# Performance work log

Measured on AMD Instinct MI355X. Metric: run time of the kernel, lower is better.

The kernel has to match this reference:

```python
import jax, jax.numpy as jnp
import numpy as np

DIM = 2048
NC = 12  # n_components (hard-coded in module)
EPS = 1e-5


def setup_inputs() -> dict:
    key = jax.random.key(0)
    ks = jax.random.split(key, 8)
    s = lambda fan_in: 1.0 / np.sqrt(fan_in)
    return {
        "x": jax.random.normal(ks[0], (8, 4096, DIM), dtype=jnp.float32),
        "Wp": jax.random.uniform(ks[1], (DIM, NC), jnp.float32, -s(DIM), s(DIM)),
        "bp": jax.random.uniform(ks[2], (NC,), jnp.float32, -s(DIM), s(DIM)),
        "Wv": jax.random.uniform(ks[3], (DIM, NC), jnp.float32, -s(DIM), s(DIM)),
        "bv": jax.random.uniform(ks[4], (NC,), jnp.float32, -s(DIM), s(DIM)),
        "Wi": jax.random.uniform(ks[5], (NC * NC, DIM), jnp.float32, -s(NC * NC), s(NC * NC)),
        "bi": jax.random.uniform(ks[6], (DIM,), jnp.float32, -s(NC * NC), s(NC * NC)),
        "gamma": jnp.ones((DIM,), jnp.float32),
        "beta": jnp.zeros((DIM,), jnp.float32),
    }


def reference(x, Wp, bp, Wv, bv, Wi, bi, gamma, beta):
    B, N, D = x.shape
    pos = x @ Wp + bp                      # [B,N,12]
    vel = x @ Wv + bv                      # [B,N,12]
    inter = jnp.einsum('bni,bnj->bnij', pos, vel).reshape(B, N, NC * NC)
    inter = inter @ Wi + bi                # [B,N,D]
    y = x + inter
    mu = jnp.mean(y, axis=-1, keepdims=True)
    var = jnp.mean(jnp.square(y - mu), axis=-1, keepdims=True)
    return (y - mu) * jax.lax.rsqrt(var + EPS) * gamma + beta
```

## Files before the change

### kernel.cpp

```cpp
#include <hip/hip_runtime.h>

#define D 2048
#define KPAD 160
#define PSTR 168
#define MTILE 16
#define THREADS 512

typedef __attribute__((ext_vector_type(8))) short bf16x8;
typedef __attribute__((ext_vector_type(4))) float f32x4;

__device__ inline unsigned short f2bf(float f) {
  unsigned int u = __float_as_uint(f);
  u += 0x7fffu + ((u >> 16) & 1u);
  return (unsigned short)(u >> 16);
}

__global__ __launch_bounds__(256) void prep_wpv(const float* __restrict__ Wp,
                                                const float* __restrict__ Wv,
                                                unsigned short* __restrict__ Wpvt) {
  int idx = blockIdx.x * 256 + threadIdx.x;
  int n = idx >> 11, k = idx & 2047;
  float v = 0.f;
  if (n < 12) v = Wp[k * 12 + n];
  else if (n < 24) v = Wv[k * 12 + (n - 12)];
  Wpvt[idx] = f2bf(v);
}

__global__ __launch_bounds__(256) void prep_wi(const float* __restrict__ Wi,
                                               unsigned short* __restrict__ Wit) {
  int idx = blockIdx.x * 256 + threadIdx.x;
  int n = idx / KPAD, k = idx - n * KPAD;
  float v = (k < 144) ? Wi[k * 2048 + n] : 0.f;
  Wit[idx] = f2bf(v);
}

__global__ __launch_bounds__(THREADS, 4) void gil_fused(
    const float* __restrict__ x, const float* __restrict__ bp,
    const float* __restrict__ bv, const float* __restrict__ bi,
    const float* __restrict__ gamma, const float* __restrict__ beta,
    const unsigned short* __restrict__ Wpvt, const unsigned short* __restrict__ Wit,
    float* __restrict__ out) {
  __shared__ float sred[8][MTILE][36];
  __shared__ __align__(16) unsigned short sP[MTILE][PSTR];
  __shared__ float spart[8][MTILE][2];
  __shared__ float sstat[MTILE][2];

  const int t = threadIdx.x;
  const int rowbase = blockIdx.x * MTILE;
  const int wave = t >> 6, lane = t & 63;
  const int lm = lane & 15, quad = lane >> 4;

  {
    const float* xr = x + (size_t)(rowbase + lm) * D + wave * 256;
    const unsigned short* b0 = Wpvt + (size_t)lm * D + wave * 256;
    const unsigned short* b1 = Wpvt + (size_t)(16 + lm) * D + wave * 256;
    f32x4 acc0 = {0.f, 0.f, 0.f, 0.f}, acc1 = {0.f, 0.f, 0.f, 0.f};
#pragma unroll
    for (int kk = 0; kk < 8; ++kk) {
      int k0 = kk * 32 + quad * 8;
      f32x4 v0 = *(const f32x4*)(xr + k0);
      f32x4 v1 = *(const f32x4*)(xr + k0 + 4);
      bf16x8 a;
#pragma unroll
      for (int e = 0; e < 4; ++e) {
        a[e]     = (short)f2bf(v0[e]);
        a[4 + e] = (short)f2bf(v1[e]);
      }
      bf16x8 w0 = *(const bf16x8*)(b0 + k0);
      bf16x8 w1 = *(const bf16x8*)(b1 + k0);
      acc0 = __builtin_amdgcn_mfma_f32_16x16x32_bf16(a, w0, acc0, 0, 0, 0);
      acc1 = __builtin_amdgcn_mfma_f32_16x16x32_bf16(a, w1, acc1, 0, 0, 0);
    }
#pragma unroll
    for (int rg = 0; rg < 4; ++rg) {
      sred[wave][quad * 4 + rg][lm]      = acc0[rg];
      sred[wave][quad * 4 + rg][16 + lm] = acc1[rg];
    }
  }
  __syncthreads();

  {
    int m = t >> 5, n = t & 31;
    float pv = 0.f;
#pragma unroll
    for (int w = 0; w < 8; ++w) pv += sred[w][m][n];
    if (n < 12) pv += bp[n];
    else if (n < 24) pv += bv[n - 12];
#pragma unroll
    for (int kk = 0; kk < 5; ++kk) {
      int k = n + 32 * kk;
      int i = k / 12, j = k - i * 12;
      float a = __shfl(pv, i, 32);
      float b = __shfl(pv, 12 + j, 32);
      sP[m][k] = f2bf((k < 144) ? a * b : 0.f);
    }
  }
  __syncthreads();

  f32x4 accv[16];
  {
    bf16x8 bf[5];
#pragma unroll
    for (int kc = 0; kc < 5; ++kc)
      bf[kc] = *(const bf16x8*)&sP[lm][kc * 32 + quad * 8];
#pragma unroll
    for (int nt = 0; nt < 16; ++nt) {
      const unsigned short* wb = Wit + (size_t)(wave * 256 + nt * 16 + lm) * KPAD;
      f32x4 acc = {0.f, 0.f, 0.f, 0.f};
#pragma unroll
      for (int kc = 0; kc < 5; ++kc) {
        bf16x8 wv = *(const bf16x8*)(wb + kc * 32 + quad * 8);
        acc = __builtin_amdgcn_mfma_f32_16x16x32_bf16(wv, bf[kc], acc, 0, 0, 0);
      }
      accv[nt] = acc;
    }
  }

  float s = 0.f, ss = 0.f;
  {
    const float* xrow = x + (size_t)(rowbase + lm) * D;
#pragma unroll
    for (int nt = 0; nt < 16; ++nt) {
      int d0 = wave * 256 + nt * 16 + quad * 4;
      f32x4 bi4 = *(const f32x4*)(bi + d0);
      f32x4 x4  = *(const f32x4*)(xrow + d0);
#pragma unroll
      for (int rg = 0; rg < 4; ++rg) {
        float y = accv[nt][rg] + bi4[rg] + x4[rg];
        accv[nt][rg] = y;
        s += y;
        ss += y * y;
      }
    }
    s += __shfl_xor(s, 16); ss += __shfl_xor(ss, 16);
    s += __shfl_xor(s, 32); ss += __shfl_xor(ss, 32);
    if (lane < 16) { spart[wave][lm][0] = s; spart[wave][lm][1] = ss; }
  }
  __syncthreads();
  if (t < MTILE) {
    float su = 0.f, sq = 0.f;
#pragma unroll
    for (int w = 0; w < 8; ++w) { su += spart[w][t][0]; sq += spart[w][t][1]; }
    float mu = su * (1.f / D);
    float var = sq * (1.f / D) - mu * mu;
    sstat[t][0] = mu;
    sstat[t][1] = rsqrtf(var + 1e-5f);
  }
  __syncthreads();

  {
    float mu = sstat[lm][0], rs = sstat[lm][1];
    float* orow = out + (size_t)(rowbase + lm) * D;
#pragma unroll
    for (int nt = 0; nt < 16; ++nt) {
      int d0 = wave * 256 + nt * 16 + quad * 4;
      f32x4 g4  = *(const f32x4*)(gamma + d0);
      f32x4 be4 = *(const f32x4*)(beta + d0);
      f32x4 o;
#pragma unroll
      for (int rg = 0; rg < 4; ++rg)
        o[rg] = (accv[nt][rg] - mu) * rs * g4[rg] + be4[rg];
      *(f32x4*)(orow + d0) = o;
    }
  }
}

extern "C" void kernel_launch(void* const* d_in, const int* in_sizes, int n_in,
                              void* d_out, int out_size, void* d_ws, size_t ws_size,
                              hipStream_t stream) {
  const float* x     = (const float*)d_in[0];
  const float* Wp    = (const float*)d_in[1];
  const float* bp    = (const float*)d_in[2];
  const float* Wv    = (const float*)d_in[3];
  const float* bv    = (const float*)d_in[4];
  const float* Wi    = (const float*)d_in[5];
  const float* bi    = (const float*)d_in[6];
  const float* gamma = (const float*)d_in[7];
  const float* beta  = (const float*)d_in[8];
  float* out = (float*)d_out;

  unsigned short* Wpvt = (unsigned short*)d_ws;
  unsigned short* Wit  = Wpvt + 32 * 2048;

  prep_wpv<<<(32 * 2048) / 256, 256, 0, stream>>>(Wp, Wv, Wpvt);
  prep_wi<<<(2048 * KPAD) / 256, 256, 0, stream>>>(Wi, Wit);

  int rows = in_sizes[0] / D;
  gil_fused<<<rows / MTILE, THREADS, 0, stream>>>(x, bp, bv, bi, gamma, beta,
                                                  Wpvt, Wit, out);
}
```

Before: 641.0 us.

## Loop each block over eight row tiles with bf16 LDS-staged x and prefetch

```diff
diff --git a/kernel.cpp b/kernel.cpp
--- a/kernel.cpp
+++ b/kernel.cpp
@@ -3,8 +3,10 @@
 #define D 2048
 #define KPAD 160
 #define PSTR 168
+#define XSTR 2072
 #define MTILE 16
-#define THREADS 512
+#define THREADS 1024
+#define NTILES 8
 
 typedef __attribute__((ext_vector_type(8))) short bf16x8;
 typedef __attribute__((ext_vector_type(4))) float f32x4;
@@ -13,6 +15,14 @@
   unsigned int u = __float_as_uint(f);
   u += 0x7fffu + ((u >> 16) & 1u);
   return (unsigned short)(u >> 16);
+}
+__device__ inline float bf2f(unsigned short h) {
+  return __uint_as_float(((unsigned int)h) << 16);
+}
+
+__device__ inline void wg_barrier() {
+  asm volatile("s_waitcnt lgkmcnt(0)" ::: "memory");
+  __builtin_amdgcn_s_barrier();
 }
 
 __global__ __launch_bounds__(256) void prep_wpv(const float* __restrict__ Wp,
@@ -40,127 +50,161 @@
     const float* __restrict__ gamma, const float* __restrict__ beta,
     const unsigned short* __restrict__ Wpvt, const unsigned short* __restrict__ Wit,
     float* __restrict__ out) {
+  __shared__ unsigned short xt[MTILE][XSTR];
   __shared__ float sred[8][MTILE][36];
   __shared__ __align__(16) unsigned short sP[MTILE][PSTR];
-  __shared__ float spart[8][MTILE][2];
+  __shared__ float spart[16][MTILE][2];
   __shared__ float sstat[MTILE][2];
+  __shared__ float sbi[D], sg[D], sb[D];
+  __shared__ float sbp_[12], sbv_[12];
 
   const int t = threadIdx.x;
-  const int rowbase = blockIdx.x * MTILE;
   const int wave = t >> 6, lane = t & 63;
   const int lm = lane & 15, quad = lane >> 4;
-
+  const int pr = t >> 6;
+  const int pc = (t & 63) * 4;
+  const int rowbase0 = blockIdx.x * (MTILE * NTILES);
+
+  for (int j = t; j < D; j += THREADS) { sbi[j] = bi[j]; sg[j] = gamma[j]; sb[j] = beta[j]; }
+  if (t < 12) { sbp_[t] = bp[t]; sbv_[t] = bv[t]; }
   {
-    const float* xr = x + (size_t)(rowbase + lm) * D + wave * 256;
-    const unsigned short* b0 = Wpvt + (size_t)lm * D + wave * 256;
-    const unsigned short* b1 = Wpvt + (size_t)(16 + lm) * D + wave * 256;
-    f32x4 acc0 = {0.f, 0.f, 0.f, 0.f}, acc1 = {0.f, 0.f, 0.f, 0.f};
-#pragma unroll
-    for (int kk = 0; kk < 8; ++kk) {
-      int k0 = kk * 32 + quad * 8;
-      f32x4 v0 = *(const f32x4*)(xr + k0);
-      f32x4 v1 = *(const f32x4*)(xr + k0 + 4);
-      bf16x8 a;
-#pragma unroll
-      for (int e = 0; e < 4; ++e) {
-        a[e]     = (short)f2bf(v0[e]);
-        a[4 + e] = (short)f2bf(v1[e]);
-      }
-      bf16x8 w0 = *(const bf16x8*)(b0 + k0);
-      bf16x8 w1 = *(const bf16x8*)(b1 + k0);
-      acc0 = __builtin_amdgcn_mfma_f32_16x16x32_bf16(a, w0, acc0, 0, 0, 0);
-      acc1 = __builtin_amdgcn_mfma_f32_16x16x32_bf16(a, w1, acc1, 0, 0, 0);
-    }
-#pragma unroll
-    for (int rg = 0; rg < 4; ++rg) {
-      sred[wave][quad * 4 + rg][lm]      = acc0[rg];
-      sred[wave][quad * 4 + rg][16 + lm] = acc1[rg];
+    const float* xp = x + (size_t)(rowbase0 + pr) * D + pc;
+    f32x4 p0[8];
+#pragma unroll
+    for (int j = 0; j < 8; ++j) p0[j] = *(const f32x4*)(xp + j * 256);
+#pragma unroll
+    for (int j = 0; j < 8; ++j) {
+      ushort4 u;
+      u.x = f2bf(p0[j][0]); u.y = f2bf(p0[j][1]);
+      u.z = f2bf(p0[j][2]); u.w = f2bf(p0[j][3]);
+      *(ushort4*)&xt[pr][pc + j * 256] = u;
     }
   }
-  __syncthreads();
-
-  {
-    int m = t >> 5, n = t & 31;
-    float pv = 0.f;
-#pragma unroll
-    for (int w = 0; w < 8; ++w) pv += sred[w][m][n];
-    if (n < 12) pv += bp[n];
-    else if (n < 24) pv += bv[n - 12];
-#pragma unroll
-    for (int kk = 0; kk < 5; ++kk) {
-      int k = n + 32 * kk;
-      int i = k / 12, j = k - i * 12;
-      float a = __shfl(pv, i, 32);
-      float b = __shfl(pv, 12 + j, 32);
-      sP[m][k] = f2bf((k < 144) ? a * b : 0.f);
-    }
-  }
-  __syncthreads();
-
-  f32x4 accv[16];
-  {
-    bf16x8 bf[5];
-#pragma unroll
-    for (int kc = 0; kc < 5; ++kc)
-      bf[kc] = *(const bf16x8*)&sP[lm][kc * 32 + quad * 8];
-#pragma unroll
-    for (int nt = 0; nt < 16; ++nt) {
-      const unsigned short* wb = Wit + (size_t)(wave * 256 + nt * 16 + lm) * KPAD;
+
+#pragma unroll 1
+  for (int it = 0; it < NTILES; ++it) {
+    const int rb = rowbase0 + it * MTILE;
+    wg_barrier();
+
+    {
+      int nt = wave & 1, ks = wave >> 1;
       f32x4 acc = {0.f, 0.f, 0.f, 0.f};
-#pragma unroll
-      for (int kc = 0; kc < 5; ++kc) {
-        bf16x8 wv = *(const bf16x8*)(wb + kc * 32 + quad * 8);
-        acc = __builtin_amdgcn_mfma_f32_16x16x32_bf16(wv, bf[kc], acc, 0, 0, 0);
-      }
-      accv[nt] = acc;
-    }
-  }
-
-  float s = 0.f, ss = 0.f;
-  {
-    const float* xrow = x + (size_t)(rowbase + lm) * D;
-#pragma unroll
-    for (int nt = 0; nt < 16; ++nt) {
-      int d0 = wave * 256 + nt * 16 + quad * 4;
-      f32x4 bi4 = *(const f32x4*)(bi + d0);
-      f32x4 x4  = *(const f32x4*)(xrow + d0);
-#pragma unroll
-      for (int rg = 0; rg < 4; ++rg) {
-        float y = accv[nt][rg] + bi4[rg] + x4[rg];
-        accv[nt][rg] = y;
-        s += y;
-        ss += y * y;
-      }
+      const unsigned short* bptr = Wpvt + (size_t)(nt * 16 + lm) * D + ks * 256;
+#pragma unroll
+      for (int kk = 0; kk < 8; ++kk) {
+        int k0 = kk * 32 + quad * 8;
+        bf16x8 a = *(const bf16x8*)&xt[lm][ks * 256 + k0];
+        bf16x8 b = *(const bf16x8*)(bptr + k0);
+        acc = __builtin_amdgcn_mfma_f32_16x16x32_bf16(a, b, acc, 0, 0, 0);
+      }
+#pragma unroll
+      for (int rg = 0; rg < 4; ++rg)
+        sred[ks][quad * 4 + rg][nt * 16 + lm] = acc[rg];
+    }
+    wg_barrier();
+
+    if (t < 512) {
+      int m = t >> 5, n = t & 31;
+      float pv = 0.f;
+#pragma unroll
+      for (int w2 = 0; w2 < 8; ++w2) pv += sred[w2][m][n];
+      if (n < 12) pv += sbp_[n];
+      else if (n < 24) pv += sbv_[n - 12];
+#pragma unroll
+      for (int kk = 0; kk < 5; ++kk) {
+        int k = n + 32 * kk;
+        int i = k / 12, j = k - i * 12;
+        float a = __shfl(pv, i, 32);
+        float b = __shfl(pv, 12 + j, 32);
+        sP[m][k] = f2bf((k < 144) ? a * b : 0.f);
+      }
+    }
+    wg_barrier();
+
+    f32x4 accv[8];
+    {
+      bf16x8 af[5];
+#pragma unroll
+      for (int kc = 0; kc < 5; ++kc)
+        af[kc] = *(const bf16x8*)&sP[lm][kc * 32 + quad * 8];
+#pragma unroll
+      for (int nt2 = 0; nt2 < 8; ++nt2) {
+        const unsigned short* wb = Wit + (size_t)(wave * 128 + nt2 * 16 + lm) * KPAD;
+        f32x4 acc = {0.f, 0.f, 0.f, 0.f};
+#pragma unroll
+        for (int kc = 0; kc < 5; ++kc) {
+          bf16x8 wv = *(const bf16x8*)(wb + kc * 32 + quad * 8);
+          acc = __builtin_amdgcn_mfma_f32_16x16x32_bf16(wv, af[kc], acc, 0, 0, 0);
+        }
+        accv[nt2] = acc;
+      }
+    }
+
+    __builtin_amdgcn_sched_barrier(0);
+    const bool havepf = (it + 1 < NTILES);
+    f32x4 pf[8];
+    if (havepf) {
+      const float* xp = x + (size_t)(rb + MTILE + pr) * D + pc;
+#pragma unroll
+      for (int j = 0; j < 8; ++j) pf[j] = *(const f32x4*)(xp + j * 256);
+    }
+
+    float s = 0.f, ss = 0.f;
+    const int dbase = wave * 128;
+#pragma unroll
+    for (int nt2 = 0; nt2 < 8; ++nt2) {
+      int d0 = dbase + nt2 * 16 + quad * 4;
+      f32x4 bi4 = *(const f32x4*)&sbi[d0];
+      ushort4 xv = *(const ushort4*)&xt[lm][d0];
+      float xf0 = bf2f(xv.x), xf1 = bf2f(xv.y), xf2 = bf2f(xv.z), xf3 = bf2f(xv.w);
+      float y0 = accv[nt2][0] + bi4[0] + xf0;
+      float y1 = accv[nt2][1] + bi4[1] + xf1;
+      float y2 = accv[nt2][2] + bi4[2] + xf2;
+      float y3 = accv[nt2][3] + bi4[3] + xf3;
+      accv[nt2][0] = y0; accv[nt2][1] = y1; accv[nt2][2] = y2; accv[nt2][3] = y3;
+      s += y0 + y1 + y2 + y3;
+      ss += y0 * y0 + y1 * y1 + y2 * y2 + y3 * y3;
     }
     s += __shfl_xor(s, 16); ss += __shfl_xor(ss, 16);
     s += __shfl_xor(s, 32); ss += __shfl_xor(ss, 32);
     if (lane < 16) { spart[wave][lm][0] = s; spart[wave][lm][1] = ss; }
-  }
-  __syncthreads();
-  if (t < MTILE) {
-    float su = 0.f, sq = 0.f;
-#pragma unroll
-    for (int w = 0; w < 8; ++w) { su += spart[w][t][0]; sq += spart[w][t][1]; }
-    float mu = su * (1.f / D);
-    float var = sq * (1.f / D) - mu * mu;
-    sstat[t][0] = mu;
-    sstat[t][1] = rsqrtf(var + 1e-5f);
-  }
-  __syncthreads();
-
-  {
-    float mu = sstat[lm][0], rs = sstat[lm][1];
-    float* orow = out + (size_t)(rowbase + lm) * D;
-#pragma unroll
-    for (int nt = 0; nt < 16; ++nt) {
-      int d0 = wave * 256 + nt * 16 + quad * 4;
-      f32x4 g4  = *(const f32x4*)(gamma + d0);
-      f32x4 be4 = *(const f32x4*)(beta + d0);
-      f32x4 o;
-#pragma unroll
-      for (int rg = 0; rg < 4; ++rg)
-        o[rg] = (accv[nt][rg] - mu) * rs * g4[rg] + be4[rg];
-      *(f32x4*)(orow + d0) = o;
+    wg_barrier();
+
+    if (t < MTILE) {
+      float su = 0.f, sq = 0.f;
+#pragma unroll
+      for (int w2 = 0; w2 < 16; ++w2) { su += spart[w2][t][0]; sq += spart[w2][t][1]; }
+      float mu = su * (1.f / D);
+      float var = sq * (1.f / D) - mu * mu;
+      sstat[t][0] = mu;
+      sstat[t][1] = rsqrtf(var + 1e-5f);
+    }
+    wg_barrier();
+
+    if (havepf) {
+#pragma unroll
+      for (int j = 0; j < 8; ++j) {
+        ushort4 u;
+        u.x = f2bf(pf[j][0]); u.y = f2bf(pf[j][1]);
+        u.z = f2bf(pf[j][2]); u.w = f2bf(pf[j][3]);
+        *(ushort4*)&xt[pr][pc + j * 256] = u;
+      }
+    }
+
+    {
+      float mu = sstat[lm][0], rs = sstat[lm][1];
+      float* orow = out + (size_t)(rb + lm) * D;
+#pragma unroll
+      for (int nt2 = 0; nt2 < 8; ++nt2) {
+        int d0 = dbase + nt2 * 16 + quad * 4;
+        f32x4 g4 = *(const f32x4*)&sg[d0];
+        f32x4 b4 = *(const f32x4*)&sb[d0];
+        f32x4 o;
+#pragma unroll
+        for (int rg = 0; rg < 4; ++rg)
+          o[rg] = (accv[nt2][rg] - mu) * rs * g4[rg] + b4[rg];
+        *(f32x4*)(orow + d0) = o;
+      }
     }
   }
 }
@@ -186,6 +230,7 @@
   prep_wi<<<(2048 * KPAD) / 256, 256, 0, stream>>>(Wi, Wit);
 
   int rows = in_sizes[0] / D;
-  gil_fused<<<rows / MTILE, THREADS, 0, stream>>>(x, bp, bv, bi, gamma, beta,
-                                                  Wpvt, Wit, out);
-}
+  int tiles = rows / MTILE;
+  gil_fused<<<tiles / NTILES, THREADS, 0, stream>>>(x, bp, bv, bi, gamma, beta,
+                                                    Wpvt, Wit, out);
+}
```

Result: slower. 689.1 us (+7.5%).
